# Optimization experiments

Hardware: AMD Instinct MI355X
Metric: run time of the kernel (lower is better)

The kernel has to match this reference:

```python
import jax, jax.numpy as jnp
import numpy as np

# Irreps config: input/output = 32x0e + 16x1o (dim 80), H=4 heads -> head = 8x0e + 4x1o (dim 20)
M0, M1 = 32, 16      # input muls for 0e / 1o
m0, m1 = 8, 4        # per-head muls
H = 4
HEAD_DIM = m0 + 3 * m1   # 20
WNUM = H * (M0 * m0 + M1 * m0 + M0 * m1 + M1 * m1)  # 2304 per-edge TP weights
NB, HID = 16, 64
SQRT3 = np.float32(np.sqrt(3.0))
EPS = 1e-8


def radial_mlp(x, W1, b1, W2, b2):
    return jax.nn.silu(x @ W1 + b1) @ W2 + b2


def tp_edge(ss, vv, sh0, sh1, w):
    """FullyConnectedTensorProduct (32x0e+16x1o) x (1x0e+1x1o) -> H*(8x0e+4x1o) with per-edge weights w [E, WNUM].
    Paths: 0e*0e->0e, 1o*1o->0e (CG dot/sqrt3), 0e*1o->1o, 1o*0e->1o; path norm 1/sqrt(fan_in)."""
    E = ss.shape[0]
    per = M0 * m0 + M1 * m0 + M0 * m1 + M1 * m1  # 576
    w = w.reshape(E, H, per)
    o = 0
    Wss = w[..., o:o + M0 * m0].reshape(E, H, M0, m0); o += M0 * m0
    Wvv = w[..., o:o + M1 * m0].reshape(E, H, M1, m0); o += M1 * m0
    Wsv = w[..., o:o + M0 * m1].reshape(E, H, M0, m1); o += M0 * m1
    Wvs = w[..., o:o + M1 * m1].reshape(E, H, M1, m1)
    fan = np.float32(np.sqrt(M0 + M1))  # fan_in = 48 for both output irreps
    vv_dot = jnp.einsum('eui,ei->eu', vv, sh1) / SQRT3
    out0 = (jnp.einsum('eu,ehuw->ehw', ss * sh0[:, None], Wss)
            + jnp.einsum('eu,ehuw->ehw', vv_dot, Wvv)) / fan          # [E,H,m0]
    out1 = (jnp.einsum('eu,ehuw->ehw', ss, Wsv)[..., None] * sh1[:, None, None, :]
            + jnp.einsum('eui,ehuw->ehwi', vv * sh0[:, None, None], Wvs)) / fan  # [E,H,m1,3]
    return out0, out1


def setup_inputs() -> dict:
    key = jax.random.key(0)
    ks = jax.random.split(key, 24)
    N, E = 2000, 32000
    g = lambda k, s, sc=1.0: jax.random.normal(k, s, jnp.float32) * sc
    inp = {}
    inp['node_features'] = g(ks[0], (N, M0 + 3 * M1))
    inp['edge_index'] = jax.random.randint(ks[1], (2, E), 0, N)
    inp['edge_sh'] = g(ks[2], (E, 4))
    inp['edge_radial_emb'] = jax.random.uniform(ks[3], (E, NB), jnp.float32)
    # query e3nn Linear (per-head blocks)
    inp['Wq0'] = g(ks[4], (H, M0, m0))
    inp['Wq1'] = g(ks[5], (H, M1, m1))
    # radial MLPs for key / value TP weights
    inp['Wk1'] = g(ks[6], (NB, HID), 1 / np.sqrt(NB)); inp['bk1'] = jnp.zeros((HID,), jnp.float32)
    inp['Wk2'] = g(ks[7], (HID, WNUM), 1 / np.sqrt(HID)); inp['bk2'] = jnp.zeros((WNUM,), jnp.float32)
    inp['Wv1'] = g(ks[8], (NB, HID), 1 / np.sqrt(NB)); inp['bv1'] = jnp.zeros((HID,), jnp.float32)
    inp['Wv2'] = g(ks[9], (HID, WNUM), 1 / np.sqrt(HID)); inp['bv2'] = jnp.zeros((WNUM,), jnp.float32)
    # single-head dot-product TP -> 0e (shared weights)
    inp['Wd0'] = g(ks[10], (m0, m0))
    inp['Wd1'] = g(ks[11], (m1, m1))
    # output projection Linear (all heads mixed per irrep)
    inp['Wo0'] = g(ks[12], (H * m0, M0))
    inp['Wo1'] = g(ks[13], (H * m1, M1))
    # FFN: out irreps -> (2*M0)x0e + M1x1o -> out irreps
    inp['Wf1_0'] = g(ks[14], (M0, 2 * M0))
    inp['Wf1_1'] = g(ks[15], (M1, M1))
    inp['Wf2_0'] = g(ks[16], (2 * M0, M0))
    inp['Wf2_1'] = g(ks[17], (M1, M1))
    return inp


def reference(node_features, edge_index, edge_sh, edge_radial_emb,
              Wq0, Wq1, Wk1, bk1, Wk2, bk2, Wv1, bv1, Wv2, bv2,
              Wd0, Wd1, Wo0, Wo1, Wf1_0, Wf1_1, Wf2_0, Wf2_1):
    N = node_features.shape[0]
    s = node_features[:, :M0]                       # [N, M0] scalars
    v = node_features[:, M0:].reshape(N, M1, 3)     # [N, M1, 3] vectors
    src, dst = edge_index[0], edge_index[1]

    # query Linear (e3nn: per-irrep channel mix, norm 1/sqrt(fan_in))
    q0 = jnp.einsum('nu,huw->nhw', s, Wq0) / np.sqrt(M0)
    q1 = jnp.einsum('nui,huw->nhwi', v, Wq1) / np.sqrt(M1)

    sh0, sh1 = edge_sh[:, 0], edge_sh[:, 1:4]
    ss, vv = s[src], v[src]                         # gather per edge

    wk = radial_mlp(edge_radial_emb, Wk1, bk1, Wk2, bk2)
    wv = radial_mlp(edge_radial_emb, Wv1, bv1, Wv2, bv2)
    k0, k1 = tp_edge(ss, vv, sh0, sh1, wk)
    v0, v1 = tp_edge(ss, vv, sh0, sh1, wv)

    # per-head equivariant dot product -> 0e logits
    qd0, qd1 = q0[dst], q1[dst]
    fan_d = np.float32(np.sqrt(m0 * m0 + m1 * m1))
    logits = (jnp.einsum('ehu,uv,ehv->eh', qd0, Wd0, k0)
              + jnp.einsum('ehui,uv,ehvi->eh', qd1, Wd1, k1) / SQRT3) / fan_d
    logits = logits / np.sqrt(HEAD_DIM)             # self.scale
    logits = jnp.clip(logits, -10.0, 10.0)

    # scatter softmax over edges sharing a destination node
    seg_max = jax.ops.segment_max(logits, dst, num_segments=N)
    seg_max = jnp.maximum(seg_max, -10.0)           # handle empty segments
    ex = jnp.exp(logits - seg_max[dst])
    denom = jax.ops.segment_sum(ex, dst, num_segments=N)
    alpha = ex / (denom[dst] + 1e-12)               # [E, H]

    agg0 = jax.ops.segment_sum(alpha[..., None] * v0, dst, num_segments=N)        # [N,H,m0]
    agg1 = jax.ops.segment_sum(alpha[..., None, None] * v1, dst, num_segments=N)  # [N,H,m1,3]

    # output projection Linear over concatenated heads
    o0 = agg0.reshape(N, H * m0) @ Wo0 / np.sqrt(H * m0)
    o1 = jnp.einsum('nui,uw->nwi', agg1.reshape(N, H * m1, 3), Wo1) / np.sqrt(H * m1)

    # residual (input irreps == output irreps -> identity skip)
    x0 = s + o0
    x1 = v + o1

    # FFN with SafeNormActivation
    f0 = x0 @ Wf1_0 / np.sqrt(M0)                               # [N, 2*M0]
    f1 = jnp.einsum('nui,uw->nwi', x1, Wf1_1) / np.sqrt(M1)     # [N, M1, 3]
    a0 = jax.nn.silu(f0)
    norms = jnp.linalg.norm(f1, axis=-1, keepdims=True)
    safe = jnp.maximum(norms, EPS)
    a1 = jnp.where(norms < EPS, 0.0, (f1 / safe) * jax.nn.silu(norms))
    g0 = a0 @ Wf2_0 / np.sqrt(2 * M0)
    g1 = jnp.einsum('nui,uw->nwi', a1, Wf2_1) / np.sqrt(M1)

    out0 = x0 + g0
    out1 = x1 + g1
    return jnp.concatenate([out0, out1.reshape(N, M1 * 3)], axis=-1)
```

## Files before the change

kernel.cpp:

```cpp
#include <hip/hip_runtime.h>

typedef unsigned int uint;
typedef unsigned short ushort;
typedef __attribute__((ext_vector_type(8))) short bf16x8;
typedef __attribute__((ext_vector_type(4))) float f32x4;
typedef __attribute__((ext_vector_type(2))) float f32x2;

#define N_NODES 2000
#define N_EDGES 32000
#define WNUM 2304

constexpr size_t OFF_AGG0 = 0;
constexpr size_t OFF_AGG1 = 64000;
constexpr size_t OFF_DEN  = 160000;
constexpr size_t OFF_CNT  = 168000;
constexpr size_t OFF_FLAG = 170000;
constexpr size_t OFF_W2T  = 170004;
constexpr size_t OFF_QT0  = 317460;
constexpr size_t OFF_QT1  = 381460;
constexpr size_t OFF_EORD = 477460;
constexpr size_t OFF_W1T  = 509460;
constexpr size_t OFF_W1P  = 511508;

__device__ __forceinline__ float b2f(ushort u){ union{uint i; float f;}x; x.i=((uint)u)<<16; return x.f; }
__device__ __forceinline__ float lo16(uint w){ union{uint u; float f;}x; x.u=w<<16; return x.f; }
__device__ __forceinline__ float hi16(uint w){ union{uint u; float f;}x; x.u=w&0xFFFF0000u; return x.f; }
__device__ __forceinline__ ushort f2b(float f){
  union{float f; uint u;}x; x.f=f;
  uint r = (x.u + 0x7FFFu + ((x.u>>16)&1u)) >> 16;
  return (ushort)r;
}
__device__ __forceinline__ float siluf(float x){ return x / (1.f + __expf(-x)); }

template<bool F32>
__device__ __forceinline__ float ldf(const void* p, int i){
  if (F32) return ((const float*)p)[i];
  return b2f(((const ushort*)p)[i]);
}
__device__ __forceinline__ float ldfr(const void* p, int i, bool f32){
  return f32 ? ((const float*)p)[i] : b2f(((const ushort*)p)[i]);
}

template<bool F32>
__device__ void prep_body(
    const void* __restrict__ nf, const int* __restrict__ eidx,
    const void* __restrict__ Wk2, const void* __restrict__ Wv2,
    const void* __restrict__ Wk1, const void* __restrict__ Wv1,
    const void* __restrict__ Wq0, const void* __restrict__ Wq1,
    const void* __restrict__ Wd0, const void* __restrict__ Wd1,
    ushort* __restrict__ W2T, float* __restrict__ W1T, uint* __restrict__ W1P,
    float* __restrict__ qt0, float* __restrict__ qt1,
    int* __restrict__ cnt){
  const int t = threadIdx.x;
  const int bid = blockIdx.x;

  if (bid < 72){
    __shared__ ushort tile[64][66];
    const int mat = bid / 36, jt = bid - mat*36;
    const void* W = mat ? Wv2 : Wk2;
    const int j0 = jt*64;
    const int jo = t & 63, cb = t >> 6;
    #pragma unroll
    for (int k=0; k<16; ++k){
      const int c = cb + k*4;
      tile[c][jo] = F32 ? f2b(((const float*)W)[(size_t)c*WNUM + j0 + jo])
                        : ((const ushort*)W)[(size_t)c*WNUM + j0 + jo];
    }
    __syncthreads();
    const int jl = t >> 2, c0 = (t & 3)*16;
    ushort* dst = W2T + (size_t)mat*147456 + (size_t)(j0+jl)*64 + c0;
    #pragma unroll
    for (int k=0; k<16; ++k) dst[k] = tile[c0+k][jl];
  } else if (bid < 104){
    __shared__ float nfL[64][80];
    __shared__ float wq0L[1024], wq1L[256], wd0L[64], wd1L[16];
    const int nb = bid - 72, n0 = nb*64;
    for (int idx=t; idx<64*80; idx+=256){
      const int nn = n0 + idx/80;
      nfL[idx/80][idx%80] = (nn < N_NODES) ? ldf<F32>(nf, nn*80 + idx%80) : 0.f;
    }
    for (int idx=t; idx<1024; idx+=256) wq0L[idx] = ldf<F32>(Wq0, idx);
    if (t < 256) wq1L[t] = ldf<F32>(Wq1, t);
    if (t < 64)  wd0L[t] = ldf<F32>(Wd0, t);
    if (t < 16)  wd1L[t] = ldf<F32>(Wd1, t);
    __syncthreads();
// ... 6 lines not shown
      for (int w=0; w<8; ++w){
        float a = 0.f;
        #pragma unroll
        for (int u=0; u<32; ++u) a += S[u]*wq0L[h*256 + u*8 + w];
        q0[w] = a * 0.17677669529663687f;
      }
      #pragma unroll
      for (int vv=0; vv<8; ++vv){
        float a = 0.f;
        #pragma unroll
        for (int u=0; u<8; ++u) a += q0[u]*wd0L[u*8+vv];
        qt0[nn*32 + h*8 + vv] = a;
      }
      float q1[12];
      #pragma unroll
      for (int w=0; w<4; ++w)
        #pragma unroll
        for (int i=0; i<3; ++i){
          float a = 0.f;
          #pragma unroll
          for (int u=0; u<16; ++u) a += S[32+u*3+i]*wq1L[h*64 + u*4 + w];
          q1[w*3+i] = a * 0.25f;
        }
      #pragma unroll
      for (int vv=0; vv<4; ++vv)
        #pragma unroll
        for (int i=0; i<3; ++i){
          float a = 0.f;
          #pragma unroll
          for (int u=0; u<4; ++u) a += q1[u*3+i]*wd1L[u*4+vv];
          qt1[nn*48 + h*12 + vv*3 + i] = a;
        }
    }
  } else if (bid == 104){
    for (int idx=t; idx<2048; idx+=256){
      const int mat = idx >> 10, rem = idx & 1023;
      const int c = rem >> 4, b = rem & 15;
      W1T[idx] = ldf<F32>(mat ? Wv1 : Wk1, b*64 + c);
    }
    for (int idx=t; idx<1024; idx+=256){
      const int mat = idx >> 9, rem = idx & 511;
      const int c = rem >> 3, j = rem & 7;
      const void* W = mat ? Wv1 : Wk1;
      ushort u0, u1;
      if (F32){ u0 = f2b(((const float*)W)[(2*j)*64+c]); u1 = f2b(((const float*)W)[(2*j+1)*64+c]); }
      else    { u0 = ((const ushort*)W)[(2*j)*64+c];     u1 = ((const ushort*)W)[(2*j+1)*64+c]; }
      W1P[idx] = (uint)u0 | ((uint)u1 << 16);
    }
  } else {
    const int e = (bid-105)*256 + t;
    if (e < N_EDGES) atomicAdd(cnt + eidx[N_EDGES + e], 1);
  }
}

__global__ __launch_bounds__(256) void prep_kernel(
    const void* nf, const int* eidx,
    const void* Wk2, const void* Wv2,
    const void* Wk1, const void* Wv1,
    const void* Wq0, const void* Wq1,
    const void* Wd0, const void* Wd1,
    ushort* W2T, float* W1T, uint* W1P, float* qt0, float* qt1,
    int* cnt, int* flag){
  __shared__ int s_cnt;
  const int t = threadIdx.x;
  if (t == 0) s_cnt = 0;
  __syncthreads();
  {
    uint u = ((const ushort*)nf)[t*2];
    uint ex = (u >> 7) & 0xFFu;
    if (ex >= 0xA0u) atomicAdd(&s_cnt, 1);
  }
  __syncthreads();
  const bool F32 = (s_cnt >= 20);
  if (blockIdx.x == 0 && t == 0) *flag = F32 ? 1 : 0;
  if (F32) prep_body<true >(nf, eidx, Wk2, Wv2, Wk1, Wv1, Wq0, Wq1, Wd0, Wd1, W2T, W1T, W1P, qt0, qt1, cnt);
  else     prep_body<false>(nf, eidx, Wk2, Wv2, Wk1, Wv1, Wq0, Wq1, Wd0, Wd1, W2T, W1T, W1P, qt0, qt1, cnt);
}

__global__ __launch_bounds__(256) void scan_kernel(int* __restrict__ cnt){
  __shared__ int ls[256];
  const int t = threadIdx.x;
  const int base = t*8;
  int v[8]; int s = 0;
  #pragma unroll
  for (int k=0; k<8; ++k){ int idx = base+k; v[k] = (idx < N_NODES) ? cnt[idx] : 0; s += v[k]; }
  ls[t] = s; __syncthreads();
  for (int off=1; off<256; off<<=1){
    int x = (t >= off) ? ls[t-off] : 0;
    __syncthreads();
    ls[t] += x;
    __syncthreads();
  }
  int ex = ls[t] - s;
  #pragma unroll
  for (int k=0; k<8; ++k){ int idx = base+k; if (idx < N_NODES){ int c = v[k]; cnt[idx] = ex; ex += c; } }
}

__global__ __launch_bounds__(256) void scat_kernel(const int* __restrict__ eidx,
                                                   int* __restrict__ cnt, int* __restrict__ eord){
  int e = blockIdx.x*256 + threadIdx.x;
  if (e < N_EDGES){
    int p = atomicAdd(cnt + eidx[N_EDGES + e], 1);
    eord[p] = e;
  }
}

struct Smem {
  ushort hidA[4096];
  union {
    struct {
      float fssT[32][34];
      float fvvT[16][34];
      float sslT[32][34];
    } f;
    float cont[2688];
  } u;
  float vshT[3][16][34];
  float sh1T[3][34];
  float exL[32][4];
  int   dstL[32];
};

__device__ __forceinline__ f32x4 mma_pair(const bf16x8& a0f, const bf16x8& a1f,
                                          bf16x8 b0, bf16x8 b1, float bb){
  f32x4 c = {bb,bb,bb,bb};
  c = __builtin_amdgcn_mfma_f32_16x16x32_bf16(a0f, b0, c, 0,0,0);
  c = __builtin_amdgcn_mfma_f32_16x16x32_bf16(a1f, b1, c, 0,0,0);
  return c;
}
__device__ __forceinline__ void acc_feat(const f32x4 c, const float* fp, float* acc){
  f32x2 fA = *(const f32x2*)(fp);
  f32x2 fB = *(const f32x2*)(fp + 2);
  acc[0] += c[0]*fA[0]; acc[1] += c[1]*fA[1];
  acc[2] += c[2]*fB[0]; acc[3] += c[3]*fB[1];
}

template<bool F32>
__device__ void edge_body(
    const void* __restrict__ nf,  const int* __restrict__ eidx,
    const int* __restrict__ eord,
    const void* __restrict__ esh, const void* __restrict__ emb,
    const float* __restrict__ W1T, const uint* __restrict__ W1P,
    const void* __restrict__ bk1, const void* __restrict__ bk2,
    const void* __restrict__ bv1, const void* __restrict__ bv2,
    const ushort* __restrict__ W2T,
    const float* __restrict__ qt0g, const float* __restrict__ qt1g,
    float* __restrict__ agg0, float* __restrict__ agg1, float* __restrict__ denom,
    Smem& sm){
  const int t  = threadIdx.x;
  const int geb = blockIdx.x*32;

  {
    const int g = t >> 5, r = t & 31;
    int geA[2], srcA[2], dstA[2];
    float shv0[2], shv1[2], shv2[2], shv3[2];
    #pragma unroll
    for (int e=0; e<2; ++e) geA[e] = eord[geb + g*2 + e];
    #pragma unroll
    for (int e=0; e<2; ++e){ srcA[e] = eidx[geA[e]]; dstA[e] = eidx[N_EDGES + geA[e]]; }
    #pragma unroll
    for (int e=0; e<2; ++e){
      if (F32){
        float4 s4 = ((const float4*)esh)[geA[e]];
        shv0[e]=s4.x; shv1[e]=s4.y; shv2[e]=s4.z; shv3[e]=s4.w;
      } else {
        uint2 u2 = ((const uint2*)esh)[geA[e]];
        shv0[e]=lo16(u2.x); shv1[e]=hi16(u2.x); shv2[e]=lo16(u2.y); shv3[e]=hi16(u2.y);
      }
    }
    #pragma unroll
    for (int e=0; e<2; ++e){
      const int le = g*2+e, src = srcA[e];
      const float sh0 = shv0[e], s1a = shv1[e], s1b = shv2[e], s1c = shv3[e];
      if (r == 0) sm.dstL[le] = dstA[e];
      if (r < 3) sm.sh1T[r][le] = (r==0)? s1a : (r==1)? s1b : s1c;
      float sv = ldf<F32>(nf, src*80 + r);
      sm.u.f.sslT[r][le] = sv;
      sm.u.f.fssT[r][le] = sv * sh0;
      if (r < 16){
        float v0 = ldf<F32>(nf, src*80+32+r*3+0);
        float v1 = ldf<F32>(nf, src*80+32+r*3+1);
        float v2 = ldf<F32>(nf, src*80+32+r*3+2);
        sm.vshT[0][r][le] = v0*sh0; sm.vshT[1][r][le] = v1*sh0; sm.vshT[2][r][le] = v2*sh0;
        sm.u.f.fvvT[r][le] = (v0*s1a + v1*s1b + v2*s1c) * 0.5773502691896258f;
      }
    }
  }

  {
    const int c  = t & 63;
    const int g4 = t >> 6;
    int geB[4];
    #pragma unroll
    for (int e=0; e<4; ++e) geB[e] = eord[geb + g4*4 + e];

    float bkv = ldf<F32>(bk1, c), bvv = ldf<F32>(bv1, c);
    f32x4 wkF[4], wvF[4];
    uint4 wkB[2], wvB[2];
    if (F32){
      const f32x4* pk = (const f32x4*)(W1T + c*16);
      const f32x4* pv = (const f32x4*)(W1T + 1024 + c*16);
      wkF[0]=pk[0]; wkF[1]=pk[1]; wkF[2]=pk[2]; wkF[3]=pk[3];
      wvF[0]=pv[0]; wvF[1]=pv[1]; wvF[2]=pv[2]; wvF[3]=pv[3];
    } else {
      const uint4* pk = (const uint4*)(W1P + c*8);
      const uint4* pv = (const uint4*)(W1P + 512 + c*8);
      wkB[0]=pk[0]; wkB[1]=pk[1];
      wvB[0]=pv[0]; wvB[1]=pv[1];
    }
    uint4 ra, rb; float4 fa, fb, fc, fd;
    if (F32){
      const float4* p = (const float4*)emb + (size_t)geB[0]*4;
      fa = p[0]; fb = p[1]; fc = p[2]; fd = p[3];
    } else {
      const uint4* p = (const uint4*)emb + (size_t)geB[0]*2;
      ra = p[0]; rb = p[1];
    }
    #pragma unroll
    for (int e=0; e<4; ++e){
      float em[16];
      if (F32){
        em[0]=fa.x; em[1]=fa.y; em[2]=fa.z; em[3]=fa.w;
        em[4]=fb.x; em[5]=fb.y; em[6]=fb.z; em[7]=fb.w;
        em[8]=fc.x; em[9]=fc.y; em[10]=fc.z; em[11]=fc.w;
        em[12]=fd.x; em[13]=fd.y; em[14]=fd.z; em[15]=fd.w;
      } else {
        em[0]=lo16(ra.x); em[1]=hi16(ra.x); em[2]=lo16(ra.y); em[3]=hi16(ra.y);
        em[4]=lo16(ra.z); em[5]=hi16(ra.z); em[6]=lo16(ra.w); em[7]=hi16(ra.w);
        em[8]=lo16(rb.x); em[9]=hi16(rb.x); em[10]=lo16(rb.y); em[11]=hi16(rb.y);
        em[12]=lo16(rb.z); em[13]=hi16(rb.z); em[14]=lo16(rb.w); em[15]=hi16(rb.w);
      }
      if (e < 3){
        if (F32){
          const float4* p = (const float4*)emb + (size_t)geB[e+1]*4;
          fa = p[0]; fb = p[1]; fc = p[2]; fd = p[3];
        } else {
          const uint4* p = (const uint4*)emb + (size_t)geB[e+1]*2;
          ra = p[0]; rb = p[1];
        }
      }
      const int le = g4*4+e;
      float ak = bkv, av = bvv;
      if (F32){
        #pragma unroll
        for (int g=0; g<4; ++g)
          #pragma unroll
          for (int j=0; j<4; ++j){
            ak += em[g*4+j]*wkF[g][j];
            av += em[g*4+j]*wvF[g][j];
          }
      } else {
        #pragma unroll
        for (int g=0; g<2; ++g){
          const uint4 a = wkB[g], b = wvB[g];
          ak += em[g*8+0]*lo16(a.x) + em[g*8+1]*hi16(a.x)
              + em[g*8+2]*lo16(a.y) + em[g*8+3]*hi16(a.y)
              + em[g*8+4]*lo16(a.z) + em[g*8+5]*hi16(a.z)
              + em[g*8+6]*lo16(a.w) + em[g*8+7]*hi16(a.w);
          av += em[g*8+0]*lo16(b.x) + em[g*8+1]*hi16(b.x)
              + em[g*8+2]*lo16(b.y) + em[g*8+3]*hi16(b.y)
              + em[g*8+4]*lo16(b.z) + em[g*8+5]*hi16(b.z)
              + em[g*8+6]*lo16(b.w) + em[g*8+7]*hi16(b.w);
        }
      }
      const int idx = (le>>4)*1024 + (c>>5)*512 + ((((c>>3)&3)*16 + (le&15))<<3) + (c&7);
      sm.hidA[idx]        = f2b(siluf(ak));
      sm.hidA[2048 + idx] = f2b(siluf(av));
    }
  }
  __syncthreads();

  const int w  = t >> 6;
  const int kv = w >> 2;
  const int h  = w & 3;
  const int lane = t & 63, q = lane >> 4, n = lane & 15;
  const float invfan = 0.14433756729740643f;

  const ushort* wptr = W2T + (size_t)kv*147456 + h*36864 + n*64 + q*8;
  const void* bvec = kv ? bv2 : bk2;
  const int bi0 = h*576 + n;
  const float* fb_ss = &sm.u.f.fssT[n>>3][q*4];
  const float* fb_sl = &sm.u.f.sslT[n>>2][q*4];
  const int nq2 = n>>2;

  bf16x8 af[2][2];
  #pragma unroll
  for (int Mt=0; Mt<2; ++Mt)
    #pragma unroll
    for (int kh=0; kh<2; ++kh)
      af[Mt][kh] = *(const bf16x8*)&sm.hidA[kv*2048 + Mt*1024 + kh*512 + lane*8];

  float a0[2][4], aP[2][4], aW[3][2][4];
  #pragma unroll
  for (int Mt=0; Mt<2; ++Mt)
    #pragma unroll
    for (int z=0; z<4; ++z){
      a0[Mt][z]=0.f; aP[Mt][z]=0.f;
      aW[0][Mt][z]=0.f; aW[1][Mt][z]=0.f; aW[2][Mt][z]=0.f;
    }

#define PREF(P0,P1,PB,TL) \
  P0 = *(const bf16x8*)(wptr + (TL)*1024); \
  P1 = *(const bf16x8*)(wptr + (TL)*1024 + 32); \
  PB = ldf<F32>(bvec, bi0 + (TL)*16);

  bf16x8 pA0, pA1, pB0, pB1; float pAb, pBb;
  PREF(pA0, pA1, pAb, 0);
  PREF(pB0, pB1, pBb, 1);

  #pragma unroll 2
  for (int tl=0; tl<24; tl+=2){
    { bf16x8 b0=pA0, b1=pA1; float bb=pAb;
      PREF(pA0, pA1, pAb, tl+2);
      const float* fp = fb_ss + tl*68;
      #pragma unroll
      for (int Mt=0; Mt<2; ++Mt) acc_feat(mma_pair(af[Mt][0], af[Mt][1], b0, b1, bb), fp + Mt*16, a0[Mt]); }
    { bf16x8 b0=pB0, b1=pB1; float bb=pBb;
      PREF(pB0, pB1, pBb, tl+3);
      const float* fp = fb_ss + (tl+1)*68;
      #pragma unroll
      for (int Mt=0; Mt<2; ++Mt) acc_feat(mma_pair(af[Mt][0], af[Mt][1], b0, b1, bb), fp + Mt*16, a0[Mt]); }
  }
  #pragma unroll 2
  for (int tl=24; tl<32; tl+=2){
    { bf16x8 b0=pA0, b1=pA1; float bb=pAb;
      PREF(pA0, pA1, pAb, tl+2);
      const float* fp = fb_sl + (tl-24)*136;
      #pragma unroll
      for (int Mt=0; Mt<2; ++Mt) acc_feat(mma_pair(af[Mt][0], af[Mt][1], b0, b1, bb), fp + Mt*16, aP[Mt]); }
    { bf16x8 b0=pB0, b1=pB1; float bb=pBb;
      PREF(pB0, pB1, pBb, tl+3);
      const float* fp = fb_sl + (tl-23)*136;
      #pragma unroll
      for (int Mt=0; Mt<2; ++Mt) acc_feat(mma_pair(af[Mt][0], af[Mt][1], b0, b1, bb), fp + Mt*16, aP[Mt]); }
  }
#define BODY_AW(B0,B1,BB,TL) { \
    const int u = ((TL)-32)*4 + nq2; \
    _Pragma("unroll") \
    for (int Mt=0; Mt<2; ++Mt){ \
      f32x4 c = mma_pair(af[Mt][0], af[Mt][1], B0, B1, BB); \
      _Pragma("unroll") \
      for (int i=0; i<3; ++i) acc_feat(c, &sm.vshT[i][u][Mt*16+q*4], aW[i][Mt]); \
    } }
  { bf16x8 b0=pA0, b1=pA1; float bb=pAb; PREF(pA0, pA1, pAb, 34); BODY_AW(b0,b1,bb,32); }
  { bf16x8 b0=pB0, b1=pB1; float bb=pBb; PREF(pB0, pB1, pBb, 35); BODY_AW(b0,b1,bb,33); }
  { bf16x8 b0=pA0, b1=pA1; float bb=pAb; BODY_AW(b0,b1,bb,34); }
  { bf16x8 b0=pB0, b1=pB1; float bb=pBb; BODY_AW(b0,b1,bb,35); }
#undef BODY_AW
#undef PREF

  #pragma unroll
  for (int Mt=0; Mt<2; ++Mt)
    #pragma unroll
    for (int z=0; z<4; ++z){
      a0[Mt][z] += __shfl_xor(a0[Mt][z], 8, 64);
      aP[Mt][z] += __shfl_xor(aP[Mt][z], 4, 64);
      aP[Mt][z] += __shfl_xor(aP[Mt][z], 8, 64);
      #pragma unroll
      for (int i=0; i<3; ++i){
        aW[i][Mt][z] += __shfl_xor(aW[i][Mt][z], 4, 64);
        aW[i][Mt][z] += __shfl_xor(aW[i][Mt][z], 8, 64);
      }
    }

  if (kv == 0){
    float lgp[2][4];
    #pragma unroll
    for (int Mt=0; Mt<2; ++Mt)
      #pragma unroll
      for (int z=0; z<4; ++z){
        const int el = Mt*16 + q*4 + z;
        const int d = sm.dstL[el];
        float acc = 0.f;
        if (n < 8) acc = qt0g[d*32 + h*8 + n] * a0[Mt][z];
        if (n < 4){
          float s = 0.f;
          #pragma unroll
          for (int i=0; i<3; ++i){
            float k1 = aP[Mt][z]*sm.sh1T[i][el] + aW[i][Mt][z];
            s += qt1g[d*48 + h*12 + n*3 + i] * k1;
          }
          acc += s * 0.5773502691896258f;
        }
        lgp[Mt][z] = acc;
      }
    #pragma unroll
    for (int Mt=0; Mt<2; ++Mt)
      #pragma unroll
      for (int z=0; z<4; ++z){
        lgp[Mt][z] += __shfl_xor(lgp[Mt][z], 1, 64);
        lgp[Mt][z] += __shfl_xor(lgp[Mt][z], 2, 64);
        lgp[Mt][z] += __shfl_xor(lgp[Mt][z], 4, 64);
        lgp[Mt][z] += __shfl_xor(lgp[Mt][z], 8, 64);
      }
    if (n == 0){
      #pragma unroll
      for (int Mt=0; Mt<2; ++Mt)
        #pragma unroll
        for (int z=0; z<4; ++z){
          float lg = lgp[Mt][z] * invfan * 0.025f;
          lg = fminf(10.f, fmaxf(-10.f, lg));
          sm.exL[Mt*16 + q*4 + z][h] = __expf(lg - 10.0f);
        }
    }
  }
  __syncthreads();

  if (kv == 1){
    #pragma unroll
    for (int Mt=0; Mt<2; ++Mt)
      #pragma unroll
      for (int z=0; z<4; ++z){
        const int el = Mt*16 + q*4 + z;
        const float ex = sm.exL[el][h];
        float* cp = &sm.u.cont[el*84 + h*21];
        if (n == 0) cp[0] = ex;
        if (n < 8)  cp[1+n] = ex * a0[Mt][z] * invfan;
        if (n < 4){
          #pragma unroll
          for (int i=0; i<3; ++i){
            float v1 = (aP[Mt][z]*sm.sh1T[i][el] + aW[i][Mt][z]) * invfan;
            cp[9+n*3+i] = ex * v1;
          }
        }
      }
  }
  __syncthreads();

  if (t < 336){
    const int quarter = t / 84;
    const int tt = t - quarter*84;
    const int h2 = tt / 21, comp = tt - h2*21;
    const int e0 = quarter*8, e1 = e0 + 8;
    float acc = 0.f;
    #pragma unroll 4
    for (int e2=e0; e2<e1; ++e2){
      acc += sm.u.cont[e2*84 + h2*21 + comp];
      const int d2 = sm.dstL[e2];
      if (e2 == e1-1 || sm.dstL[e2+1] != d2){
        if (comp == 0)      atomicAdd(denom + d2*4  + h2, acc);
        else if (comp < 9)  atomicAdd(agg0  + d2*32 + h2*8  + (comp-1), acc);
        else                atomicAdd(agg1  + d2*48 + h2*12 + (comp-9), acc);
        acc = 0.f;
      }
    }
  }
}

__global__ __launch_bounds__(512) void edge_kernel(
    const void* nf, const int* eidx, const int* eord, const void* esh, const void* emb,
    const float* W1T, const uint* W1P,
    const void* bk1, const void* bk2,
    const void* bv1, const void* bv2,
    const ushort* W2T, const float* qt0g, const float* qt1g,
    float* agg0, float* agg1, float* denom, const int* flag){
  __shared__ Smem sm;
  if (*flag)
    edge_body<true >(nf,eidx,eord,esh,emb,W1T,W1P,bk1,bk2,bv1,bv2,W2T,qt0g,qt1g,agg0,agg1,denom,sm);
  else
    edge_body<false>(nf,eidx,eord,esh,emb,W1T,W1P,bk1,bk2,bv1,bv2,W2T,qt0g,qt1g,agg0,agg1,denom,sm);
}

__global__ __launch_bounds__(256) void node_out_kernel(
    const void* __restrict__ nf, const float* __restrict__ agg0r, const float* __restrict__ agg1r,
    const float* __restrict__ denom,
    const void* __restrict__ Wo0, const void* __restrict__ Wo1,
    const void* __restrict__ Wf10, const void* __restrict__ Wf11,
    const void* __restrict__ Wf20, const void* __restrict__ Wf21,
    void* __restrict__ out, const int* __restrict__ flag){
  __shared__ float ag0[4][32], ag1[4][48], adiv[4][4];
  __shared__ float x0s[4][32], x1s[4][48], a0s[4][64], f1s[4][48], coefs[4][16];
  const bool F32 = (*flag) != 0;
  const int s = threadIdx.x >> 6, t = threadIdx.x & 63;
  const int n = blockIdx.x*4 + s;
  if (t < 4) adiv[s][t] = 1.f / (denom[n*4+t] + 1e-12f);
  __syncthreads();
  if (t < 32) ag0[s][t] = agg0r[n*32+t] * adiv[s][t>>3];
  if (t < 48) ag1[s][t] = agg1r[n*48+t] * adiv[s][t/12];
  __syncthreads();
  if (t < 32){
    float o = 0.f;
    #pragma unroll
    for (int k=0; k<32; ++k) o += ag0[s][k]*ldfr(Wo0, k*32+t, F32);
    x0s[s][t] = ldfr(nf, n*80+t, F32) + o*0.17677669529663687f;
  }
  if (t < 48){
    int w = t/3, i = t - w*3;
    float o = 0.f;
    #pragma unroll
    for (int u=0; u<16; ++u) o += ag1[s][u*3+i]*ldfr(Wo1, u*16+w, F32);
    x1s[s][t] = ldfr(nf, n*80+32+t, F32) + o*0.25f;
  }
  __syncthreads();
// ... 35 lines not shown
  }
}

extern "C" void kernel_launch(void* const* d_in, const int* in_sizes, int n_in,
                              void* d_out, int out_size, void* d_ws, size_t ws_size,
                              hipStream_t stream){
  const void* nf   = d_in[0];
  const int*  eidx = (const int*)d_in[1];
  const void* esh  = d_in[2];
  const void* emb  = d_in[3];
  const void* Wq0  = d_in[4];
  const void* Wq1  = d_in[5];
  const void* Wk1  = d_in[6];
  const void* bk1  = d_in[7];
  const void* Wk2  = d_in[8];
  const void* bk2  = d_in[9];
  const void* Wv1  = d_in[10];
  const void* bv1  = d_in[11];
  const void* Wv2  = d_in[12];
  const void* bv2  = d_in[13];
  const void* Wd0  = d_in[14];
  const void* Wd1  = d_in[15];
  const void* Wo0  = d_in[16];
  const void* Wo1  = d_in[17];
  const void* Wf10 = d_in[18];
  const void* Wf11 = d_in[19];
  const void* Wf20 = d_in[20];
  const void* Wf21 = d_in[21];
  float* ws = (float*)d_ws;

  float* agg0  = ws + OFF_AGG0;
  float* agg1  = ws + OFF_AGG1;
  float* denom = ws + OFF_DEN;
  int*   cnt   = (int*)(ws + OFF_CNT);
  int*   flag  = (int*)(ws + OFF_FLAG);
  ushort* W2T  = (ushort*)(ws + OFF_W2T);
  float* qt0   = ws + OFF_QT0;
  float* qt1   = ws + OFF_QT1;
  int*   eord  = (int*)(ws + OFF_EORD);
  float* W1T   = ws + OFF_W1T;
  uint*  W1P   = (uint*)(ws + OFF_W1P);

  hipMemsetAsync(agg0, 0, 170000*sizeof(float), stream);
  prep_kernel<<<230, 256, 0, stream>>>(nf, eidx, Wk2, Wv2, Wk1, Wv1, Wq0, Wq1, Wd0, Wd1,
                                       W2T, W1T, W1P, qt0, qt1, cnt, flag);
  scan_kernel<<<1, 256, 0, stream>>>(cnt);
  scat_kernel<<<125, 256, 0, stream>>>(eidx, cnt, eord);
  edge_kernel<<<N_EDGES/32, 512, 0, stream>>>(nf, eidx, eord, esh, emb,
                                              W1T, W1P, bk1, bk2, bv1, bv2,
                                              W2T, qt0, qt1,
                                              agg0, agg1, denom, flag);
  node_out_kernel<<<N_NODES/4, 256, 0, stream>>>(nf, agg0, agg1, denom,
                                                 Wo0, Wo1, Wf10, Wf11, Wf20, Wf21, d_out, flag);
}
```

Measured before the change: 235.5 us.

## Drop edge sorting by destination and halve edge-kernel block size

Removes the counting-sort pipeline (count atomics in prep, scan kernel, scatter kernel) so edges are processed in original order, and every component of every edge is atomically added to the aggregates directly instead of being run-length reduced over equal destinations. The edge kernel now uses 256 threads per block, and each wave computes both the key and value tensor-product halves in a loop, keeping exp logits in registers rather than shared memory. This removes two kernel launches and the sort work, but raises the number of global atomics and may increase contention and per-wave serial work.

```diff
diff --git a/kernel.cpp b/kernel.cpp
--- a/kernel.cpp
+++ b/kernel.cpp
@@ -13,12 +13,10 @@
 constexpr size_t OFF_AGG0 = 0;
 constexpr size_t OFF_AGG1 = 64000;
 constexpr size_t OFF_DEN  = 160000;
-constexpr size_t OFF_CNT  = 168000;
 constexpr size_t OFF_FLAG = 170000;
 constexpr size_t OFF_W2T  = 170004;
 constexpr size_t OFF_QT0  = 317460;
 constexpr size_t OFF_QT1  = 381460;
-constexpr size_t OFF_EORD = 477460;
 constexpr size_t OFF_W1T  = 509460;
 constexpr size_t OFF_W1P  = 511508;
 
@@ -43,14 +41,13 @@
 
 template<bool F32>
 __device__ void prep_body(
-    const void* __restrict__ nf, const int* __restrict__ eidx,
+    const void* __restrict__ nf,
     const void* __restrict__ Wk2, const void* __restrict__ Wv2,
     const void* __restrict__ Wk1, const void* __restrict__ Wv1,
     const void* __restrict__ Wq0, const void* __restrict__ Wq1,
     const void* __restrict__ Wd0, const void* __restrict__ Wd1,
     ushort* __restrict__ W2T, float* __restrict__ W1T, uint* __restrict__ W1P,
-    float* __restrict__ qt0, float* __restrict__ qt1,
-    int* __restrict__ cnt){
+    float* __restrict__ qt0, float* __restrict__ qt1){
   const int t = threadIdx.x;
   const int bid = blockIdx.x;
 
@@ -123,7 +120,7 @@
           qt1[nn*48 + h*12 + vv*3 + i] = a;
         }
     }
-  } else if (bid == 104){
+  } else {
     for (int idx=t; idx<2048; idx+=256){
       const int mat = idx >> 10, rem = idx & 1023;
       const int c = rem >> 4, b = rem & 15;
@@ -138,20 +135,17 @@
       else    { u0 = ((const ushort*)W)[(2*j)*64+c];     u1 = ((const ushort*)W)[(2*j+1)*64+c]; }
       W1P[idx] = (uint)u0 | ((uint)u1 << 16);
     }
-  } else {
-    const int e = (bid-105)*256 + t;
-    if (e < N_EDGES) atomicAdd(cnt + eidx[N_EDGES + e], 1);
   }
 }
 
 __global__ __launch_bounds__(256) void prep_kernel(
-    const void* nf, const int* eidx,
+    const void* nf,
     const void* Wk2, const void* Wv2,
     const void* Wk1, const void* Wv1,
     const void* Wq0, const void* Wq1,
     const void* Wd0, const void* Wd1,
     ushort* W2T, float* W1T, uint* W1P, float* qt0, float* qt1,
-    int* cnt, int* flag){
+    int* flag){
   __shared__ int s_cnt;
   const int t = threadIdx.x;
   if (t == 0) s_cnt = 0;
@@ -164,36 +158,8 @@
   __syncthreads();
   const bool F32 = (s_cnt >= 20);
   if (blockIdx.x == 0 && t == 0) *flag = F32 ? 1 : 0;
-  if (F32) prep_body<true >(nf, eidx, Wk2, Wv2, Wk1, Wv1, Wq0, Wq1, Wd0, Wd1, W2T, W1T, W1P, qt0, qt1, cnt);
-  else     prep_body<false>(nf, eidx, Wk2, Wv2, Wk1, Wv1, Wq0, Wq1, Wd0, Wd1, W2T, W1T, W1P, qt0, qt1, cnt);
-}
-
-__global__ __launch_bounds__(256) void scan_kernel(int* __restrict__ cnt){
-  __shared__ int ls[256];
-  const int t = threadIdx.x;
-  const int base = t*8;
-  int v[8]; int s = 0;
-  #pragma unroll
-  for (int k=0; k<8; ++k){ int idx = base+k; v[k] = (idx < N_NODES) ? cnt[idx] : 0; s += v[k]; }
-  ls[t] = s; __syncthreads();
-  for (int off=1; off<256; off<<=1){
-    int x = (t >= off) ? ls[t-off] : 0;
-    __syncthreads();
-    ls[t] += x;
-    __syncthreads();
-  }
-  int ex = ls[t] - s;
-  #pragma unroll
-  for (int k=0; k<8; ++k){ int idx = base+k; if (idx < N_NODES){ int c = v[k]; cnt[idx] = ex; ex += c; } }
-}
-
-__global__ __launch_bounds__(256) void scat_kernel(const int* __restrict__ eidx,
-                                                   int* __restrict__ cnt, int* __restrict__ eord){
-  int e = blockIdx.x*256 + threadIdx.x;
-  if (e < N_EDGES){
-    int p = atomicAdd(cnt + eidx[N_EDGES + e], 1);
-    eord[p] = e;
-  }
+  if (F32) prep_body<true >(nf, Wk2, Wv2, Wk1, Wv1, Wq0, Wq1, Wd0, Wd1, W2T, W1T, W1P, qt0, qt1);
+  else     prep_body<false>(nf, Wk2, Wv2, Wk1, Wv1, Wq0, Wq1, Wd0, Wd1, W2T, W1T, W1P, qt0, qt1);
 }
 
 struct Smem {
@@ -208,7 +174,6 @@
   } u;
   float vshT[3][16][34];
   float sh1T[3][34];
-  float exL[32][4];
   int   dstL[32];
 };
 
@@ -229,7 +194,6 @@
 template<bool F32>
 __device__ void edge_body(
     const void* __restrict__ nf,  const int* __restrict__ eidx,
-    const int* __restrict__ eord,
     const void* __restrict__ esh, const void* __restrict__ emb,
     const float* __restrict__ W1T, const uint* __restrict__ W1P,
     const void* __restrict__ bk1, const void* __restrict__ bk2,
@@ -239,72 +203,70 @@
     float* __restrict__ agg0, float* __restrict__ agg1, float* __restrict__ denom,
     Smem& sm){
   const int t  = threadIdx.x;
+  const int hw = t >> 5;
+  const int r  = t & 31;
   const int geb = blockIdx.x*32;
 
+  int geA[4], srcA[4], dstA[4];
+  float shv0[4], shv1[4], shv2[4], shv3[4];
+  #pragma unroll
+  for (int e=0; e<4; ++e) geA[e] = geb + hw*4 + e;
+  #pragma unroll
+  for (int e=0; e<4; ++e){ srcA[e] = eidx[geA[e]]; dstA[e] = eidx[N_EDGES + geA[e]]; }
+  #pragma unroll
+  for (int e=0; e<4; ++e){
+    if (F32){
+      float4 s4 = ((const float4*)esh)[geA[e]];
+      shv0[e]=s4.x; shv1[e]=s4.y; shv2[e]=s4.z; shv3[e]=s4.w;
+    } else {
+      uint2 u2 = ((const uint2*)esh)[geA[e]];
+      shv0[e]=lo16(u2.x); shv1[e]=hi16(u2.x); shv2[e]=lo16(u2.y); shv3[e]=hi16(u2.y);
+    }
+  }
+  #pragma unroll
+  for (int e=0; e<4; ++e){
+    const int le = hw*4+e, src = srcA[e];
+    const float sh0 = shv0[e], s1a = shv1[e], s1b = shv2[e], s1c = shv3[e];
+    if (r == 0) sm.dstL[le] = dstA[e];
+    if (r < 3) sm.sh1T[r][le] = (r==0)? s1a : (r==1)? s1b : s1c;
+    float sv = ldf<F32>(nf, src*80 + r);
+    sm.u.f.sslT[r][le] = sv;
+    sm.u.f.fssT[r][le] = sv * sh0;
+    if (r < 16){
+      float v0 = ldf<F32>(nf, src*80+32+r*3+0);
+      float v1 = ldf<F32>(nf, src*80+32+r*3+1);
+      float v2 = ldf<F32>(nf, src*80+32+r*3+2);
+      sm.vshT[0][r][le] = v0*sh0; sm.vshT[1][r][le] = v1*sh0; sm.vshT[2][r][le] = v2*sh0;
+      sm.u.f.fvvT[r][le] = (v0*s1a + v1*s1b + v2*s1c) * 0.5773502691896258f;
+    }
+  }
+
   {
-    const int g = t >> 5, r = t & 31;
-    int geA[2], srcA[2], dstA[2];
-    float shv0[2], shv1[2], shv2[2], shv3[2];
-    #pragma unroll
-    for (int e=0; e<2; ++e) geA[e] = eord[geb + g*2 + e];
-    #pragma unroll
-    for (int e=0; e<2; ++e){ srcA[e] = eidx[geA[e]]; dstA[e] = eidx[N_EDGES + geA[e]]; }
-    #pragma unroll
-    for (int e=0; e<2; ++e){
+    float bkv[2], bvv[2];
+    f32x4 wkF[2][4], wvF[2][4];
+    uint4 wkB[2][2], wvB[2][2];
+    #pragma unroll
+    for (int cc=0; cc<2; ++cc){
+      const int c = r + cc*32;
+      bkv[cc] = ldf<F32>(bk1, c); bvv[cc] = ldf<F32>(bv1, c);
       if (F32){
-        float4 s4 = ((const float4*)esh)[geA[e]];
-        shv0[e]=s4.x; shv1[e]=s4.y; shv2[e]=s4.z; shv3[e]=s4.w;
+        const f32x4* pk = (const f32x4*)(W1T + c*16);
+        const f32x4* pv = (const f32x4*)(W1T + 1024 + c*16);
+        wkF[cc][0]=pk[0]; wkF[cc][1]=pk[1]; wkF[cc][2]=pk[2]; wkF[cc][3]=pk[3];
+        wvF[cc][0]=pv[0]; wvF[cc][1]=pv[1]; wvF[cc][2]=pv[2]; wvF[cc][3]=pv[3];
       } else {
-        uint2 u2 = ((const uint2*)esh)[geA[e]];
-        shv0[e]=lo16(u2.x); shv1[e]=hi16(u2.x); shv2[e]=lo16(u2.y); shv3[e]=hi16(u2.y);
-      }
-    }
-    #pragma unroll
-    for (int e=0; e<2; ++e){
-      const int le = g*2+e, src = srcA[e];
-      const float sh0 = shv0[e], s1a = shv1[e], s1b = shv2[e], s1c = shv3[e];
-      if (r == 0) sm.dstL[le] = dstA[e];
-      if (r < 3) sm.sh1T[r][le] = (r==0)? s1a : (r==1)? s1b : s1c;
-      float sv = ldf<F32>(nf, src*80 + r);
-      sm.u.f.sslT[r][le] = sv;
-      sm.u.f.fssT[r][le] = sv * sh0;
-      if (r < 16){
-        float v0 = ldf<F32>(nf, src*80+32+r*3+0);
-        float v1 = ldf<F32>(nf, src*80+32+r*3+1);
-        float v2 = ldf<F32>(nf, src*80+32+r*3+2);
-        sm.vshT[0][r][le] = v0*sh0; sm.vshT[1][r][le] = v1*sh0; sm.vshT[2][r][le] = v2*sh0;
-        sm.u.f.fvvT[r][le] = (v0*s1a + v1*s1b + v2*s1c) * 0.5773502691896258f;
-      }
-    }
-  }
-
-  {
-    const int c  = t & 63;
-    const int g4 = t >> 6;
-    int geB[4];
-    #pragma unroll
-    for (int e=0; e<4; ++e) geB[e] = eord[geb + g4*4 + e];
-
-    float bkv = ldf<F32>(bk1, c), bvv = ldf<F32>(bv1, c);
-    f32x4 wkF[4], wvF[4];
-    uint4 wkB[2], wvB[2];
-    if (F32){
-      const f32x4* pk = (const f32x4*)(W1T + c*16);
-      const f32x4* pv = (const f32x4*)(W1T + 1024 + c*16);
-      wkF[0]=pk[0]; wkF[1]=pk[1]; wkF[2]=pk[2]; wkF[3]=pk[3];
-      wvF[0]=pv[0]; wvF[1]=pv[1]; wvF[2]=pv[2]; wvF[3]=pv[3];
-    } else {
-      const uint4* pk = (const uint4*)(W1P + c*8);
-      const uint4* pv = (const uint4*)(W1P + 512 + c*8);
-      wkB[0]=pk[0]; wkB[1]=pk[1];
-      wvB[0]=pv[0]; wvB[1]=pv[1];
+        const uint4* pk = (const uint4*)(W1P + c*8);
+        const uint4* pv = (const uint4*)(W1P + 512 + c*8);
+        wkB[cc][0]=pk[0]; wkB[cc][1]=pk[1];
+        wvB[cc][0]=pv[0]; wvB[cc][1]=pv[1];
+      }
     }
     uint4 ra, rb; float4 fa, fb, fc, fd;
     if (F32){
-      const float4* p = (const float4*)emb + (size_t)geB[0]*4;
+      const float4* p = (const float4*)emb + (size_t)geA[0]*4;
       fa = p[0]; fb = p[1]; fc = p[2]; fd = p[3];
     } else {
-      const uint4* p = (const uint4*)emb + (size_t)geB[0]*2;
+      const uint4* p = (const uint4*)emb + (size_t)geA[0]*2;
       ra = p[0]; rb = p[1];
     }
     #pragma unroll
@@ -323,108 +285,114 @@
       }
       if (e < 3){
         if (F32){
-          const float4* p = (const float4*)emb + (size_t)geB[e+1]*4;
+          const float4* p = (const float4*)emb + (size_t)geA[e+1]*4;
           fa = p[0]; fb = p[1]; fc = p[2]; fd = p[3];
         } else {
-          const uint4* p = (const uint4*)emb + (size_t)geB[e+1]*2;
+          const uint4* p = (const uint4*)emb + (size_t)geA[e+1]*2;
           ra = p[0]; rb = p[1];
         }
       }
-      const int le = g4*4+e;
-      float ak = bkv, av = bvv;
-      if (F32){
-        #pragma unroll
-        for (int g=0; g<4; ++g)
+      const int le = hw*4+e;
+      #pragma unroll
+      for (int cc=0; cc<2; ++cc){
+        const int c = r + cc*32;
+        float ak = bkv[cc], av = bvv[cc];
+        if (F32){
           #pragma unroll
-          for (int j=0; j<4; ++j){
-            ak += em[g*4+j]*wkF[g][j];
-            av += em[g*4+j]*wvF[g][j];
+          for (int g=0; g<4; ++g)
+            #pragma unroll
+            for (int j=0; j<4; ++j){
+              ak += em[g*4+j]*wkF[cc][g][j];
+              av += em[g*4+j]*wvF[cc][g][j];
+            }
+        } else {
+          #pragma unroll
+          for (int g=0; g<2; ++g){
+            const uint4 a = wkB[cc][g], b = wvB[cc][g];
+            ak += em[g*8+0]*lo16(a.x) + em[g*8+1]*hi16(a.x)
+                + em[g*8+2]*lo16(a.y) + em[g*8+3]*hi16(a.y)
+                + em[g*8+4]*lo16(a.z) + em[g*8+5]*hi16(a.z)
+                + em[g*8+6]*lo16(a.w) + em[g*8+7]*hi16(a.w);
+            av += em[g*8+0]*lo16(b.x) + em[g*8+1]*hi16(b.x)
+                + em[g*8+2]*lo16(b.y) + em[g*8+3]*hi16(b.y)
+                + em[g*8+4]*lo16(b.z) + em[g*8+5]*hi16(b.z)
+                + em[g*8+6]*lo16(b.w) + em[g*8+7]*hi16(b.w);
           }
-      } else {
-        #pragma unroll
-        for (int g=0; g<2; ++g){
-          const uint4 a = wkB[g], b = wvB[g];
-          ak += em[g*8+0]*lo16(a.x) + em[g*8+1]*hi16(a.x)
-              + em[g*8+2]*lo16(a.y) + em[g*8+3]*hi16(a.y)
-              + em[g*8+4]*lo16(a.z) + em[g*8+5]*hi16(a.z)
-              + em[g*8+6]*lo16(a.w) + em[g*8+7]*hi16(a.w);
-          av += em[g*8+0]*lo16(b.x) + em[g*8+1]*hi16(b.x)
-              + em[g*8+2]*lo16(b.y) + em[g*8+3]*hi16(b.y)
-              + em[g*8+4]*lo16(b.z) + em[g*8+5]*hi16(b.z)
-              + em[g*8+6]*lo16(b.w) + em[g*8+7]*hi16(b.w);
-        }
-      }
-      const int idx = (le>>4)*1024 + (c>>5)*512 + ((((c>>3)&3)*16 + (le&15))<<3) + (c&7);
-      sm.hidA[idx]        = f2b(siluf(ak));
-      sm.hidA[2048 + idx] = f2b(siluf(av));
-    }
-  }
-  __syncthreads();
-
-  const int w  = t >> 6;
-  const int kv = w >> 2;
-  const int h  = w & 3;
+        }
+        const int idx = (le>>4)*1024 + (c>>5)*512 + ((((c>>3)&3)*16 + (le&15))<<3) + (c&7);
+        sm.hidA[idx]        = f2b(siluf(ak));
+        sm.hidA[2048 + idx] = f2b(siluf(av));
+      }
+    }
+  }
+  __syncthreads();
+
+  const int h = t >> 6;
   const int lane = t & 63, q = lane >> 4, n = lane & 15;
   const float invfan = 0.14433756729740643f;
-
-  const ushort* wptr = W2T + (size_t)kv*147456 + h*36864 + n*64 + q*8;
-  const void* bvec = kv ? bv2 : bk2;
+  float exv[2][4];
+
+  const ushort* wbase = W2T + h*36864 + n*64 + q*8;
   const int bi0 = h*576 + n;
   const float* fb_ss = &sm.u.f.fssT[n>>3][q*4];
   const float* fb_sl = &sm.u.f.sslT[n>>2][q*4];
   const int nq2 = n>>2;
 
-  bf16x8 af[2][2];
-  #pragma unroll
-  for (int Mt=0; Mt<2; ++Mt)
-    #pragma unroll
-    for (int kh=0; kh<2; ++kh)
-      af[Mt][kh] = *(const bf16x8*)&sm.hidA[kv*2048 + Mt*1024 + kh*512 + lane*8];
-
-  float a0[2][4], aP[2][4], aW[3][2][4];
-  #pragma unroll
-  for (int Mt=0; Mt<2; ++Mt)
-    #pragma unroll
-    for (int z=0; z<4; ++z){
-      a0[Mt][z]=0.f; aP[Mt][z]=0.f;
-      aW[0][Mt][z]=0.f; aW[1][Mt][z]=0.f; aW[2][Mt][z]=0.f;
-    }
+  #pragma unroll 1
+  for (int kv=0; kv<2; ++kv){
+    const ushort* wptr = wbase + kv*147456;
+    const void* bvec = kv ? bv2 : bk2;
+    bf16x8 af[2][2];
+    #pragma unroll
+    for (int Mt=0; Mt<2; ++Mt)
+      #pragma unroll
+      for (int kh=0; kh<2; ++kh)
+        af[Mt][kh] = *(const bf16x8*)&sm.hidA[kv*2048 + Mt*1024 + kh*512 + lane*8];
+
+    float a0[2][4], aP[2][4], aW[3][2][4];
+    #pragma unroll
+    for (int Mt=0; Mt<2; ++Mt)
+      #pragma unroll
+      for (int z=0; z<4; ++z){
+        a0[Mt][z]=0.f; aP[Mt][z]=0.f;
+        aW[0][Mt][z]=0.f; aW[1][Mt][z]=0.f; aW[2][Mt][z]=0.f;
+      }
 
 #define PREF(P0,P1,PB,TL) \
   P0 = *(const bf16x8*)(wptr + (TL)*1024); \
   P1 = *(const bf16x8*)(wptr + (TL)*1024 + 32); \
   PB = ldf<F32>(bvec, bi0 + (TL)*16);
 
-  bf16x8 pA0, pA1, pB0, pB1; float pAb, pBb;
-  PREF(pA0, pA1, pAb, 0);
-  PREF(pB0, pB1, pBb, 1);
-
-  #pragma unroll 2
-  for (int tl=0; tl<24; tl+=2){
-    { bf16x8 b0=pA0, b1=pA1; float bb=pAb;
-      PREF(pA0, pA1, pAb, tl+2);
-      const float* fp = fb_ss + tl*68;
-      #pragma unroll
-      for (int Mt=0; Mt<2; ++Mt) acc_feat(mma_pair(af[Mt][0], af[Mt][1], b0, b1, bb), fp + Mt*16, a0[Mt]); }
-    { bf16x8 b0=pB0, b1=pB1; float bb=pBb;
-      PREF(pB0, pB1, pBb, tl+3);
-      const float* fp = fb_ss + (tl+1)*68;
-      #pragma unroll
-      for (int Mt=0; Mt<2; ++Mt) acc_feat(mma_pair(af[Mt][0], af[Mt][1], b0, b1, bb), fp + Mt*16, a0[Mt]); }
-  }
-  #pragma unroll 2
-  for (int tl=24; tl<32; tl+=2){
-    { bf16x8 b0=pA0, b1=pA1; float bb=pAb;
-      PREF(pA0, pA1, pAb, tl+2);
-      const float* fp = fb_sl + (tl-24)*136;
-      #pragma unroll
-      for (int Mt=0; Mt<2; ++Mt) acc_feat(mma_pair(af[Mt][0], af[Mt][1], b0, b1, bb), fp + Mt*16, aP[Mt]); }
-    { bf16x8 b0=pB0, b1=pB1; float bb=pBb;
-      PREF(pB0, pB1, pBb, tl+3);
-      const float* fp = fb_sl + (tl-23)*136;
-      #pragma unroll
-      for (int Mt=0; Mt<2; ++Mt) acc_feat(mma_pair(af[Mt][0], af[Mt][1], b0, b1, bb), fp + Mt*16, aP[Mt]); }
-  }
+    bf16x8 pA0, pA1, pB0, pB1; float pAb, pBb;
+    PREF(pA0, pA1, pAb, 0);
+    PREF(pB0, pB1, pBb, 1);
+
+    #pragma unroll 2
+    for (int tl=0; tl<24; tl+=2){
+      { bf16x8 b0=pA0, b1=pA1; float bb=pAb;
+        PREF(pA0, pA1, pAb, tl+2);
+        const float* fp = fb_ss + tl*68;
+        #pragma unroll
+        for (int Mt=0; Mt<2; ++Mt) acc_feat(mma_pair(af[Mt][0], af[Mt][1], b0, b1, bb), fp + Mt*16, a0[Mt]); }
+      { bf16x8 b0=pB0, b1=pB1; float bb=pBb;
+        PREF(pB0, pB1, pBb, tl+3);
+        const float* fp = fb_ss + (tl+1)*68;
+        #pragma unroll
+        for (int Mt=0; Mt<2; ++Mt) acc_feat(mma_pair(af[Mt][0], af[Mt][1], b0, b1, bb), fp + Mt*16, a0[Mt]); }
+    }
+    #pragma unroll 2
+    for (int tl=24; tl<32; tl+=2){
+      { bf16x8 b0=pA0, b1=pA1; float bb=pAb;
+        PREF(pA0, pA1, pAb, tl+2);
+        const float* fp = fb_sl + (tl-24)*136;
+        #pragma unroll
+        for (int Mt=0; Mt<2; ++Mt) acc_feat(mma_pair(af[Mt][0], af[Mt][1], b0, b1, bb), fp + Mt*16, aP[Mt]); }
+      { bf16x8 b0=pB0, b1=pB1; float bb=pBb;
+        PREF(pB0, pB1, pBb, tl+3);
+        const float* fp = fb_sl + (tl-23)*136;
+        #pragma unroll
+        for (int Mt=0; Mt<2; ++Mt) acc_feat(mma_pair(af[Mt][0], af[Mt][1], b0, b1, bb), fp + Mt*16, aP[Mt]); }
+    }
 #define BODY_AW(B0,B1,BB,TL) { \
     const int u = ((TL)-32)*4 + nq2; \
     _Pragma("unroll") \
@@ -433,113 +401,102 @@
       _Pragma("unroll") \
       for (int i=0; i<3; ++i) acc_feat(c, &sm.vshT[i][u][Mt*16+q*4], aW[i][Mt]); \
     } }
-  { bf16x8 b0=pA0, b1=pA1; float bb=pAb; PREF(pA0, pA1, pAb, 34); BODY_AW(b0,b1,bb,32); }
-  { bf16x8 b0=pB0, b1=pB1; float bb=pBb; PREF(pB0, pB1, pBb, 35); BODY_AW(b0,b1,bb,33); }
-  { bf16x8 b0=pA0, b1=pA1; float bb=pAb; BODY_AW(b0,b1,bb,34); }
-  { bf16x8 b0=pB0, b1=pB1; float bb=pBb; BODY_AW(b0,b1,bb,35); }
+    { bf16x8 b0=pA0, b1=pA1; float bb=pAb; PREF(pA0, pA1, pAb, 34); BODY_AW(b0,b1,bb,32); }
+    { bf16x8 b0=pB0, b1=pB1; float bb=pBb; PREF(pB0, pB1, pBb, 35); BODY_AW(b0,b1,bb,33); }
+    { bf16x8 b0=pA0, b1=pA1; float bb=pAb; BODY_AW(b0,b1,bb,34); }
+    { bf16x8 b0=pB0, b1=pB1; float bb=pBb; BODY_AW(b0,b1,bb,35); }
 #undef BODY_AW
 #undef PREF
 
-  #pragma unroll
-  for (int Mt=0; Mt<2; ++Mt)
-    #pragma unroll
-    for (int z=0; z<4; ++z){
-      a0[Mt][z] += __shfl_xor(a0[Mt][z], 8, 64);
-      aP[Mt][z] += __shfl_xor(aP[Mt][z], 4, 64);
-      aP[Mt][z] += __shfl_xor(aP[Mt][z], 8, 64);
-      #pragma unroll
-      for (int i=0; i<3; ++i){
-        aW[i][Mt][z] += __shfl_xor(aW[i][Mt][z], 4, 64);
-        aW[i][Mt][z] += __shfl_xor(aW[i][Mt][z], 8, 64);
-      }
-    }
-
-  if (kv == 0){
-    float lgp[2][4];
     #pragma unroll
     for (int Mt=0; Mt<2; ++Mt)
       #pragma unroll
       for (int z=0; z<4; ++z){
-        const int el = Mt*16 + q*4 + z;
-        const int d = sm.dstL[el];
-        float acc = 0.f;
-        if (n < 8) acc = qt0g[d*32 + h*8 + n] * a0[Mt][z];
-        if (n < 4){
-          float s = 0.f;
-          #pragma unroll
-          for (int i=0; i<3; ++i){
-            float k1 = aP[Mt][z]*sm.sh1T[i][el] + aW[i][Mt][z];
-            s += qt1g[d*48 + h*12 + n*3 + i] * k1;
+        a0[Mt][z] += __shfl_xor(a0[Mt][z], 8, 64);
+        aP[Mt][z] += __shfl_xor(aP[Mt][z], 4, 64);
+        aP[Mt][z] += __shfl_xor(aP[Mt][z], 8, 64);
+        #pragma unroll
+        for (int i=0; i<3; ++i){
+          aW[i][Mt][z] += __shfl_xor(aW[i][Mt][z], 4, 64);
+          aW[i][Mt][z] += __shfl_xor(aW[i][Mt][z], 8, 64);
+        }
+      }
+
+    if (kv == 0){
+      float lgp[2][4];
+      #pragma unroll
+      for (int Mt=0; Mt<2; ++Mt)
+        #pragma unroll
+        for (int z=0; z<4; ++z){
+          const int el = Mt*16 + q*4 + z;
+          const int d = sm.dstL[el];
+          float acc = 0.f;
+          if (n < 8) acc = qt0g[d*32 + h*8 + n] * a0[Mt][z];
+          if (n < 4){
+            float s = 0.f;
+            #pragma unroll
+            for (int i=0; i<3; ++i){
+              float k1 = aP[Mt][z]*sm.sh1T[i][el] + aW[i][Mt][z];
+              s += qt1g[d*48 + h*12 + n*3 + i] * k1;
+            }
+            acc += s * 0.5773502691896258f;
           }
-          acc += s * 0.5773502691896258f;
-        }
-        lgp[Mt][z] = acc;
-      }
-    #pragma unroll
-    for (int Mt=0; Mt<2; ++Mt)
-      #pragma unroll
-      for (int z=0; z<4; ++z){
-        lgp[Mt][z] += __shfl_xor(lgp[Mt][z], 1, 64);
-        lgp[Mt][z] += __shfl_xor(lgp[Mt][z], 2, 64);
-        lgp[Mt][z] += __shfl_xor(lgp[Mt][z], 4, 64);
-        lgp[Mt][z] += __shfl_xor(lgp[Mt][z], 8, 64);
-      }
-    if (n == 0){
+          lgp[Mt][z] = acc;
+        }
       #pragma unroll
       for (int Mt=0; Mt<2; ++Mt)
         #pragma unroll
         for (int z=0; z<4; ++z){
+          lgp[Mt][z] += __shfl_xor(lgp[Mt][z], 1, 64);
+          lgp[Mt][z] += __shfl_xor(lgp[Mt][z], 2, 64);
+          lgp[Mt][z] += __shfl_xor(lgp[Mt][z], 4, 64);
+          lgp[Mt][z] += __shfl_xor(lgp[Mt][z], 8, 64);
           float lg = lgp[Mt][z] * invfan * 0.025f;
           lg = fminf(10.f, fmaxf(-10.f, lg));
-          sm.exL[Mt*16 + q*4 + z][h] = __expf(lg - 10.0f);
-        }
-    }
-  }
-  __syncthreads();
-
-  if (kv == 1){
-    #pragma unroll
-    for (int Mt=0; Mt<2; ++Mt)
-      #pragma unroll
-      for (int z=0; z<4; ++z){
-        const int el = Mt*16 + q*4 + z;
-        const float ex = sm.exL[el][h];
-        float* cp = &sm.u.cont[el*84 + h*21];
-        if (n == 0) cp[0] = ex;
-        if (n < 8)  cp[1+n] = ex * a0[Mt][z] * invfan;
-        if (n < 4){
-          #pragma unroll
-          for (int i=0; i<3; ++i){
-            float v1 = (aP[Mt][z]*sm.sh1T[i][el] + aW[i][Mt][z]) * invfan;
-            cp[9+n*3+i] = ex * v1;
+          exv[Mt][z] = __expf(lg - 10.0f);
+        }
+    } else {
+      __syncthreads();
+      #pragma unroll
+      for (int Mt=0; Mt<2; ++Mt)
+        #pragma unroll
+        for (int z=0; z<4; ++z){
+          const int el = Mt*16 + q*4 + z;
+          const float ex = exv[Mt][z];
+          float* cp = &sm.u.cont[el*84 + h*21];
+          if (n == 0) cp[0] = ex;
+          if (n < 8)  cp[1+n] = ex * a0[Mt][z] * invfan;
+          if (n < 4){
+            #pragma unroll
+            for (int i=0; i<3; ++i){
+              float v1 = (aP[Mt][z]*sm.sh1T[i][el] + aW[i][Mt][z]) * invfan;
+              cp[9+n*3+i] = ex * v1;
+            }
           }
         }
-      }
-  }
-  __syncthreads();
-
-  if (t < 336){
-    const int quarter = t / 84;
-    const int tt = t - quarter*84;
-    const int h2 = tt / 21, comp = tt - h2*21;
-    const int e0 = quarter*8, e1 = e0 + 8;
-    float acc = 0.f;
-    #pragma unroll 4
-    for (int e2=e0; e2<e1; ++e2){
-      acc += sm.u.cont[e2*84 + h2*21 + comp];
-      const int d2 = sm.dstL[e2];
-      if (e2 == e1-1 || sm.dstL[e2+1] != d2){
-        if (comp == 0)      atomicAdd(denom + d2*4  + h2, acc);
-        else if (comp < 9)  atomicAdd(agg0  + d2*32 + h2*8  + (comp-1), acc);
-        else                atomicAdd(agg1  + d2*48 + h2*12 + (comp-9), acc);
-        acc = 0.f;
-      }
-    }
-  }
-}
-
-__global__ __launch_bounds__(512) void edge_kernel(
-    const void* nf, const int* eidx, const int* eord, const void* esh, const void* emb,
+    }
+  }
+  __syncthreads();
+
+  #pragma unroll
+  for (int k=0; k<11; ++k){
+    const int idx = t + k*256;
+    if (idx < 2688){
+      const int el = idx / 84;
+      const int cm = idx - el*84;
+      const int h2 = cm / 21;
+      const int comp = cm - h2*21;
+      const float val = sm.u.cont[idx];
+      const int d2 = sm.dstL[el];
+      if (comp == 0)      atomicAdd(denom + d2*4  + h2, val);
+      else if (comp < 9)  atomicAdd(agg0  + d2*32 + h2*8  + (comp-1), val);
+      else                atomicAdd(agg1  + d2*48 + h2*12 + (comp-9), val);
+    }
+  }
+}
+
+__global__ __launch_bounds__(256) void edge_kernel(
+    const void* nf, const int* eidx, const void* esh, const void* emb,
     const float* W1T, const uint* W1P,
     const void* bk1, const void* bk2,
     const void* bv1, const void* bv2,
@@ -547,9 +504,9 @@
     float* agg0, float* agg1, float* denom, const int* flag){
   __shared__ Smem sm;
   if (*flag)
-    edge_body<true >(nf,eidx,eord,esh,emb,W1T,W1P,bk1,bk2,bv1,bv2,W2T,qt0g,qt1g,agg0,agg1,denom,sm);
+    edge_body<true >(nf,eidx,esh,emb,W1T,W1P,bk1,bk2,bv1,bv2,W2T,qt0g,qt1g,agg0,agg1,denom,sm);
   else
-    edge_body<false>(nf,eidx,eord,esh,emb,W1T,W1P,bk1,bk2,bv1,bv2,W2T,qt0g,qt1g,agg0,agg1,denom,sm);
+    edge_body<false>(nf,eidx,esh,emb,W1T,W1P,bk1,bk2,bv1,bv2,W2T,qt0g,qt1g,agg0,agg1,denom,sm);
 }
 
 __global__ __launch_bounds__(256) void node_out_kernel(
@@ -651,21 +608,17 @@
   float* agg0  = ws + OFF_AGG0;
   float* agg1  = ws + OFF_AGG1;
   float* denom = ws + OFF_DEN;
-  int*   cnt   = (int*)(ws + OFF_CNT);
   int*   flag  = (int*)(ws + OFF_FLAG);
   ushort* W2T  = (ushort*)(ws + OFF_W2T);
   float* qt0   = ws + OFF_QT0;
   float* qt1   = ws + OFF_QT1;
-  int*   eord  = (int*)(ws + OFF_EORD);
   float* W1T   = ws + OFF_W1T;
   uint*  W1P   = (uint*)(ws + OFF_W1P);
 
-  hipMemsetAsync(agg0, 0, 170000*sizeof(float), stream);
-  prep_kernel<<<230, 256, 0, stream>>>(nf, eidx, Wk2, Wv2, Wk1, Wv1, Wq0, Wq1, Wd0, Wd1,
-                                       W2T, W1T, W1P, qt0, qt1, cnt, flag);
-  scan_kernel<<<1, 256, 0, stream>>>(cnt);
-  scat_kernel<<<125, 256, 0, stream>>>(eidx, cnt, eord);
-  edge_kernel<<<N_EDGES/32, 512, 0, stream>>>(nf, eidx, eord, esh, emb,
+  hipMemsetAsync(agg0, 0, 168000*sizeof(float), stream);
+  prep_kernel<<<105, 256, 0, stream>>>(nf, Wk2, Wv2, Wk1, Wv1, Wq0, Wq1, Wd0, Wd1,
+                                       W2T, W1T, W1P, qt0, qt1, flag);
+  edge_kernel<<<N_EDGES/32, 256, 0, stream>>>(nf, eidx, esh, emb,
                                               W1T, W1P, bk1, bk2, bv1, bv2,
                                               W2T, qt0, qt1,
                                               agg0, agg1, denom, flag);
```

Result: faster. 219.9 us (-6.6%).
